# Kernel tuning notes

Hardware: AMD Instinct MI355X
Metric: run time of the kernel (lower is better)

The kernel has to match this reference:

```python
import jax, jax.numpy as jnp
import numpy as np

TEMPERATURE = 1.0
NEG_INF = -1e30  # finite stand-in for -inf: safe for log_softmax and its vjp


def setup_inputs() -> dict:
    key = jax.random.key(0)
    k1, k2 = jax.random.split(key)
    B, M, D = 4096, 3, 256
    tokens = jax.random.normal(k1, (B, M, D), dtype=jnp.float32)
    labels = jax.random.randint(k2, (B,), 0, 32, dtype=jnp.int32)
    return {"tokens": tokens, "labels": labels}


def reference(tokens, labels):
    # tokens: [B, M, D]; labels: [B]
    B, M, D = tokens.shape
    # Pairwise per-modality similarities: sim[i, k, m] = <tokens[i,m], tokens[k,m]>
    sim = jnp.einsum('imd,kmd->ikm', tokens, tokens) / TEMPERATURE
    self_mask = jnp.eye(B, dtype=bool)
    # Original excludes sample i itself from the candidate set; masking with a
    # huge negative logit makes it contribute 0 to the softmax partition.
    sim = jnp.where(self_mask[:, :, None], NEG_INF, sim)
    logp = jax.nn.log_softmax(sim, axis=1)  # softmax over the B-1 other samples

    # Positive pairs: same label, excluding self.
    pos = (labels[:, None] == labels[None, :]) & ~self_mask  # [B, B]
    pos_count = pos.sum(axis=1)                               # [B]
    valid = pos_count > 0                                     # sum(same_label) > 1

    # Mean log-prob over positives, per (sample, modality).
    pos_logp = jnp.einsum('ikm,ik->im', logp, pos.astype(logp.dtype))  # [B, M]
    denom = jnp.maximum(pos_count, 1).astype(logp.dtype)[:, None]
    per = jnp.where(valid[:, None], pos_logp / denom, 0.0)             # [B, M]

    num = valid.sum() * M
    return -per.sum() / num.astype(per.dtype)
```

## Files before the change

kernel.cpp:

```cpp
#include <hip/hip_runtime.h>

#define B_N 4096
#define M_N 3
#define D_N 256
#define LOG2E 1.44269504088896340736f
#define LN2   0.69314718055994530942f
#define C_OFF   64.0f
#define T_CLAMP 112.0f

typedef __bf16 bf16x8 __attribute__((ext_vector_type(8)));
typedef float  f32x4  __attribute__((ext_vector_type(4)));

__device__ __forceinline__ unsigned short f2bf(float f) {
    unsigned int u = __float_as_uint(f);
    u += 0x7FFFu + ((u >> 16) & 1u);
    return (unsigned short)(u >> 16);
}
__device__ __forceinline__ float bf2f(unsigned short h) {
    return __uint_as_float(((unsigned int)h) << 16);
}

__global__ void cvt_kernel(const float* __restrict__ in, unsigned short* __restrict__ out,
                           float* __restrict__ norm2) {
    int idx = blockIdx.x * blockDim.x + threadIdx.x;
    float4 v = reinterpret_cast<const float4*>(in)[idx];
    int i   = idx / 192;
    int rem = idx - i * 192;
    int m   = rem >> 6;
    int d4  = rem & 63;
    ushort4 o;
    o.x = f2bf(v.x); o.y = f2bf(v.y); o.z = f2bf(v.z); o.w = f2bf(v.w);
    reinterpret_cast<ushort4*>(out)[((size_t)m * B_N + i) * 64 + d4] = o;
    float nx = bf2f(o.x), ny = bf2f(o.y), nz = bf2f(o.z), nw = bf2f(o.w);
    float s = nx * nx + ny * ny + nz * nz + nw * nw;
#pragma unroll
    for (int msk = 1; msk < 64; msk <<= 1) s += __shfl_xor(s, msk);
    if ((threadIdx.x & 63) == 0) norm2[m * B_N + i] = s;
}

__global__ void hist_kernel(const int* __restrict__ labels, int* __restrict__ hist,
                            int* __restrict__ nvout) {
    __shared__ int h[32];
    __shared__ int nv;
    int tid = threadIdx.x;
    if (tid < 32) h[tid] = 0;
    if (tid == 0) nv = 0;
    __syncthreads();
    for (int i = tid; i < B_N; i += 256) atomicAdd(&h[labels[i]], 1);
    __syncthreads();
    int cnt = 0;
    for (int i = tid; i < B_N; i += 256) cnt += (h[labels[i]] >= 2) ? 1 : 0;
    atomicAdd(&nv, cnt);
    __syncthreads();
    if (tid < 32) hist[tid] = h[tid];
    if (tid == 0) nvout[0] = nv;
}

__global__ __launch_bounds__(256, 3) void main_kernel(
    const unsigned short* __restrict__ tokb, const int* __restrict__ labels,
    float2* __restrict__ partials) {
    int raw = blockIdx.x;
    int bid = (raw & 7) * 96 + (raw >> 3);
    int m  = bid >> 8;
    int ns = (bid >> 5) & 7;
    int rb = bid & 31;
    int i0 = rb * 128;
    int cb = ns * 512;

    int tid  = threadIdx.x;
    int wave = tid >> 6, lane = tid & 63;
    int lr = lane & 15, lk = lane >> 4;
    const unsigned short* tm = tokb + (size_t)m * (B_N * D_N);

    __shared__ __align__(16) char ldsB[2][8192];
    __shared__ int labl[512];
    labl[tid]       = labels[cb + tid];
    labl[tid + 256] = labels[cb + tid + 256];

    int r0 = i0 + wave * 32;
    bf16x8 afrag[2][8];
#pragma unroll
    for (int rt = 0; rt < 2; ++rt) {
        const unsigned short* rp = tm + (size_t)(r0 + rt * 16 + lr) * D_N + lk * 8;
#pragma unroll
        for (int kf = 0; kf < 8; ++kf)
            afrag[rt][kf] = *reinterpret_cast<const bf16x8*>(rp + kf * 32);
    }
    int labr[2][4];
#pragma unroll
    for (int rt = 0; rt < 2; ++rt)
#pragma unroll
        for (int j = 0; j < 4; ++j)
            labr[rt][j] = labels[r0 + rt * 16 + lk * 4 + j];

    float S[2][4] = {{0.f, 0.f, 0.f, 0.f}, {0.f, 0.f, 0.f, 0.f}};
    float P[2][4] = {{0.f, 0.f, 0.f, 0.f}, {0.f, 0.f, 0.f, 0.f}};

    int lc  = tid >> 5;
    int w   = tid & 31;
    int sch = w ^ (lc & 7);
    const unsigned short* sbase = tm + (size_t)(cb + lc) * D_N + sch * 8;

    {
        bf16x8 t0 = *reinterpret_cast<const bf16x8*>(sbase);
        bf16x8 t1 = *reinterpret_cast<const bf16x8*>(sbase + 8 * D_N);
        *reinterpret_cast<bf16x8*>(&ldsB[0][tid * 16])        = t0;
        *reinterpret_cast<bf16x8*>(&ldsB[0][4096 + tid * 16]) = t1;
    }

    for (int kb = 0; kb < 32; ++kb) {
        int cur = kb & 1;
        __syncthreads();

        int nkb = (kb + 1) & 31;
        const unsigned short* np = sbase + (size_t)nkb * (16 * D_N);
        bf16x8 nt0 = *reinterpret_cast<const bf16x8*>(np);
        bf16x8 nt1 = *reinterpret_cast<const bf16x8*>(np + 8 * D_N);

        const char* bp = ldsB[cur];
        int swz = (lr & 7) << 4;
        bf16x8 bfrag[8];
#pragma unroll
        for (int kf = 0; kf < 8; ++kf)
            bfrag[kf] = *reinterpret_cast<const bf16x8*>(
                bp + lr * 512 + ((((kf * 4 + lk) << 4)) ^ swz));
        int labc = labl[kb * 16 + lr];

        f32x4 acc0 = {0.f, 0.f, 0.f, 0.f};
        f32x4 acc1 = {0.f, 0.f, 0.f, 0.f};
#pragma unroll
        for (int kf = 0; kf < 8; ++kf) {
            acc0 = __builtin_amdgcn_mfma_f32_16x16x32_bf16(afrag[0][kf], bfrag[kf], acc0, 0, 0, 0);
            acc1 = __builtin_amdgcn_mfma_f32_16x16x32_bf16(afrag[1][kf], bfrag[kf], acc1, 0, 0, 0);
        }

        int cg0 = cb + kb * 16;
        if ((cg0 < r0 + 32) && (cg0 + 16 > r0)) {
            int colg = cg0 + lr;
#pragma unroll
            for (int rt = 0; rt < 2; ++rt) {
                f32x4 aa = rt ? acc1 : acc0;
#pragma unroll
                for (int j = 0; j < 4; ++j) {
                    float s = aa[j];
                    float t = fminf(fmaf(s, LOG2E, -C_OFF), T_CLAMP);
                    float e = __builtin_amdgcn_exp2f(t);
                    int row = r0 + rt * 16 + lk * 4 + j;
                    e = (colg == row) ? 0.f : e;
                    S[rt][j] += e;
                    P[rt][j] += (labc == labr[rt][j]) ? s : 0.f;
                }
            }
        } else {
#pragma unroll
            for (int rt = 0; rt < 2; ++rt) {
                f32x4 aa = rt ? acc1 : acc0;
#pragma unroll
                for (int j = 0; j < 4; ++j) {
                    float s = aa[j];
                    float t = fminf(fmaf(s, LOG2E, -C_OFF), T_CLAMP);
                    S[rt][j] += __builtin_amdgcn_exp2f(t);
                    P[rt][j] += (labc == labr[rt][j]) ? s : 0.f;
                }
            }
        }

        char* dst = (char*)ldsB[cur ^ 1];
        *reinterpret_cast<bf16x8*>(dst + tid * 16)        = nt0;
        *reinterpret_cast<bf16x8*>(dst + 4096 + tid * 16) = nt1;
    }

#pragma unroll
    for (int rt = 0; rt < 2; ++rt)
#pragma unroll
        for (int j = 0; j < 4; ++j) {
            float sv = S[rt][j], pv = P[rt][j];
#pragma unroll
            for (int msk = 1; msk < 16; msk <<= 1) {
                sv += __shfl_xor(sv, msk);
                pv += __shfl_xor(pv, msk);
            }
            if (lr == 0) {
                int rl = rt * 16 + lk * 4 + j;
                float2 q; q.x = sv; q.y = pv;
                partials[(size_t)(((m * 32 + rb) * 8 + ns) * 128) + wave * 32 + rl] = q;
            }
        }
}

__global__ void reduce_kernel(const float2* __restrict__ partials,
                              const float* __restrict__ norm2,
                              const int* __restrict__ labels,
                              const int* __restrict__ hist,
                              float* __restrict__ blockpart) {
    int gid = blockIdx.x * 256 + threadIdx.x;
    int m = gid >> 12, i = gid & 4095;
    int rb = i >> 7, r = i & 127;
    const float2* pp = partials + (size_t)(((m * 32 + rb) * 8) * 128) + r;
    float S = 0.f, P = 0.f;
#pragma unroll
    for (int ns = 0; ns < 8; ++ns) {
        float2 q = pp[ns * 128];
        S += q.x; P += q.y;
    }
    P -= norm2[gid];
    int pc = hist[labels[i]] - 1;
    float contrib = (pc > 0)
        ? (__builtin_amdgcn_logf(S) + C_OFF) * LN2 - P / (float)pc
        : 0.f;
#pragma unroll
    for (int off = 32; off >= 1; off >>= 1) contrib += __shfl_down(contrib, off);
    __shared__ float w4[4];
    if ((threadIdx.x & 63) == 0) w4[threadIdx.x >> 6] = contrib;
    __syncthreads();
    if (threadIdx.x == 0) blockpart[blockIdx.x] = w4[0] + w4[1] + w4[2] + w4[3];
}

__global__ void final_kernel(const float* __restrict__ blockpart, const int* __restrict__ nv,
                             float* __restrict__ out) {
    int lane = threadIdx.x;
    float s = (lane < 48) ? blockpart[lane] : 0.f;
#pragma unroll
    for (int off = 32; off >= 1; off >>= 1) s += __shfl_down(s, off);
    if (lane == 0) out[0] = s / (float)(nv[0] * M_N);
}

extern "C" void kernel_launch(void* const* d_in, const int* in_sizes, int n_in,
                              void* d_out, int out_size, void* d_ws, size_t ws_size,
                              hipStream_t stream) {
    const float* tokens = (const float*)d_in[0];
    const int*   labels = (const int*)d_in[1];
    float* out = (float*)d_out;

    char* ws = (char*)d_ws;
    int*    hist      = (int*)ws;
    int*    nv        = (int*)(ws + 128);
    float*  blockpart = (float*)(ws + 256);
    float*  norm2     = (float*)(ws + 1024);
    float2* partials  = (float2*)(ws + 65536);
    unsigned short* tokb = (unsigned short*)(ws + 1048576);

    cvt_kernel<<<3072, 256, 0, stream>>>(tokens, tokb, norm2);
    hist_kernel<<<1, 256, 0, stream>>>(labels, hist, nv);
    main_kernel<<<768, 256, 0, stream>>>(tokb, labels, partials);
    reduce_kernel<<<48, 256, 0, stream>>>(partials, norm2, labels, hist, blockpart);
    final_kernel<<<1, 64, 0, stream>>>(blockpart, nv, out);
}
```

Before: 56.91 us.

## Double LDS stage depth, add MFMA priority, drop exp clamp, widen hist block

The main kernel now stages 32 columns per LDS phase instead of 16, which halves the number of barriers per block and issues four global loads per thread per phase. It raises wave priority around the MFMA chains with s_setprio. It also removes the fminf clamp before exp2, and the histogram kernel runs with 1024 threads. Together these aim to cut barrier and instruction overhead, at the cost of doubled LDS use and a possible overflow if a similarity exceeds the clamp range.

```diff
diff --git a/kernel.cpp b/kernel.cpp
--- a/kernel.cpp
+++ b/kernel.cpp
@@ -5,8 +5,7 @@
 #define D_N 256
 #define LOG2E 1.44269504088896340736f
 #define LN2   0.69314718055994530942f
-#define C_OFF   64.0f
-#define T_CLAMP 112.0f
+#define C_OFF 64.0f
 
 typedef __bf16 bf16x8 __attribute__((ext_vector_type(8)));
 typedef float  f32x4  __attribute__((ext_vector_type(4)));
@@ -46,10 +45,10 @@
     if (tid < 32) h[tid] = 0;
     if (tid == 0) nv = 0;
     __syncthreads();
-    for (int i = tid; i < B_N; i += 256) atomicAdd(&h[labels[i]], 1);
+    for (int i = tid; i < B_N; i += 1024) atomicAdd(&h[labels[i]], 1);
     __syncthreads();
     int cnt = 0;
-    for (int i = tid; i < B_N; i += 256) cnt += (h[labels[i]] >= 2) ? 1 : 0;
+    for (int i = tid; i < B_N; i += 1024) cnt += (h[labels[i]] >= 2) ? 1 : 0;
     atomicAdd(&nv, cnt);
     __syncthreads();
     if (tid < 32) hist[tid] = h[tid];
@@ -72,7 +71,7 @@
     int lr = lane & 15, lk = lane >> 4;
     const unsigned short* tm = tokb + (size_t)m * (B_N * D_N);
 
-    __shared__ __align__(16) char ldsB[2][8192];
+    __shared__ __align__(16) char ldsB[2][16384];
     __shared__ int labl[512];
     labl[tid]       = labels[cb + tid];
     labl[tid + 256] = labels[cb + tid + 256];
@@ -104,70 +103,82 @@
     {
         bf16x8 t0 = *reinterpret_cast<const bf16x8*>(sbase);
         bf16x8 t1 = *reinterpret_cast<const bf16x8*>(sbase + 8 * D_N);
-        *reinterpret_cast<bf16x8*>(&ldsB[0][tid * 16])        = t0;
-        *reinterpret_cast<bf16x8*>(&ldsB[0][4096 + tid * 16]) = t1;
-    }
-
-    for (int kb = 0; kb < 32; ++kb) {
-        int cur = kb & 1;
+        bf16x8 t2 = *reinterpret_cast<const bf16x8*>(sbase + 16 * D_N);
+        bf16x8 t3 = *reinterpret_cast<const bf16x8*>(sbase + 24 * D_N);
+        *reinterpret_cast<bf16x8*>(&ldsB[0][tid * 16])         = t0;
+        *reinterpret_cast<bf16x8*>(&ldsB[0][4096 + tid * 16])  = t1;
+        *reinterpret_cast<bf16x8*>(&ldsB[0][8192 + tid * 16])  = t2;
+        *reinterpret_cast<bf16x8*>(&ldsB[0][12288 + tid * 16]) = t3;
+    }
+
+    for (int ph = 0; ph < 16; ++ph) {
+        int cur = ph & 1;
         __syncthreads();
 
-        int nkb = (kb + 1) & 31;
-        const unsigned short* np = sbase + (size_t)nkb * (16 * D_N);
+        int nph = (ph + 1) & 15;
+        const unsigned short* np = sbase + (size_t)nph * (32 * D_N);
         bf16x8 nt0 = *reinterpret_cast<const bf16x8*>(np);
         bf16x8 nt1 = *reinterpret_cast<const bf16x8*>(np + 8 * D_N);
+        bf16x8 nt2 = *reinterpret_cast<const bf16x8*>(np + 16 * D_N);
+        bf16x8 nt3 = *reinterpret_cast<const bf16x8*>(np + 24 * D_N);
 
         const char* bp = ldsB[cur];
         int swz = (lr & 7) << 4;
-        bf16x8 bfrag[8];
-#pragma unroll
-        for (int kf = 0; kf < 8; ++kf)
-            bfrag[kf] = *reinterpret_cast<const bf16x8*>(
-                bp + lr * 512 + ((((kf * 4 + lk) << 4)) ^ swz));
-        int labc = labl[kb * 16 + lr];
-
-        f32x4 acc0 = {0.f, 0.f, 0.f, 0.f};
-        f32x4 acc1 = {0.f, 0.f, 0.f, 0.f};
-#pragma unroll
-        for (int kf = 0; kf < 8; ++kf) {
-            acc0 = __builtin_amdgcn_mfma_f32_16x16x32_bf16(afrag[0][kf], bfrag[kf], acc0, 0, 0, 0);
-            acc1 = __builtin_amdgcn_mfma_f32_16x16x32_bf16(afrag[1][kf], bfrag[kf], acc1, 0, 0, 0);
+#pragma unroll
+        for (int s = 0; s < 2; ++s) {
+            bf16x8 bfrag[8];
+#pragma unroll
+            for (int kf = 0; kf < 8; ++kf)
+                bfrag[kf] = *reinterpret_cast<const bf16x8*>(
+                    bp + (s * 16 + lr) * 512 + (((kf * 4 + lk) << 4) ^ swz));
+            int kb = ph * 2 + s;
+            int labc = labl[kb * 16 + lr];
+
+            f32x4 acc0 = {0.f, 0.f, 0.f, 0.f};
+            f32x4 acc1 = {0.f, 0.f, 0.f, 0.f};
+            __builtin_amdgcn_s_setprio(1);
+#pragma unroll
+            for (int kf = 0; kf < 8; ++kf) {
+                acc0 = __builtin_amdgcn_mfma_f32_16x16x32_bf16(afrag[0][kf], bfrag[kf], acc0, 0, 0, 0);
+                acc1 = __builtin_amdgcn_mfma_f32_16x16x32_bf16(afrag[1][kf], bfrag[kf], acc1, 0, 0, 0);
+            }
+            __builtin_amdgcn_s_setprio(0);
+
+            int cg0 = cb + kb * 16;
+            if ((cg0 < r0 + 32) && (cg0 + 16 > r0)) {
+                int colg = cg0 + lr;
+#pragma unroll
+                for (int rt = 0; rt < 2; ++rt) {
+                    f32x4 aa = rt ? acc1 : acc0;
+#pragma unroll
+                    for (int j = 0; j < 4; ++j) {
+                        float s2 = aa[j];
+                        float e = __builtin_amdgcn_exp2f(fmaf(s2, LOG2E, -C_OFF));
+                        int row = r0 + rt * 16 + lk * 4 + j;
+                        e = (colg == row) ? 0.f : e;
+                        S[rt][j] += e;
+                        P[rt][j] += (labc == labr[rt][j]) ? s2 : 0.f;
+                    }
+                }
+            } else {
+#pragma unroll
+                for (int rt = 0; rt < 2; ++rt) {
+                    f32x4 aa = rt ? acc1 : acc0;
+#pragma unroll
+                    for (int j = 0; j < 4; ++j) {
+                        float s2 = aa[j];
+                        S[rt][j] += __builtin_amdgcn_exp2f(fmaf(s2, LOG2E, -C_OFF));
+                        P[rt][j] += (labc == labr[rt][j]) ? s2 : 0.f;
+                    }
+                }
+            }
         }
 
-        int cg0 = cb + kb * 16;
-        if ((cg0 < r0 + 32) && (cg0 + 16 > r0)) {
-            int colg = cg0 + lr;
-#pragma unroll
-            for (int rt = 0; rt < 2; ++rt) {
-                f32x4 aa = rt ? acc1 : acc0;
-#pragma unroll
-                for (int j = 0; j < 4; ++j) {
-                    float s = aa[j];
-                    float t = fminf(fmaf(s, LOG2E, -C_OFF), T_CLAMP);
-                    float e = __builtin_amdgcn_exp2f(t);
-                    int row = r0 + rt * 16 + lk * 4 + j;
-                    e = (colg == row) ? 0.f : e;
-                    S[rt][j] += e;
-                    P[rt][j] += (labc == labr[rt][j]) ? s : 0.f;
-                }
-            }
-        } else {
-#pragma unroll
-            for (int rt = 0; rt < 2; ++rt) {
-                f32x4 aa = rt ? acc1 : acc0;
-#pragma unroll
-                for (int j = 0; j < 4; ++j) {
-                    float s = aa[j];
-                    float t = fminf(fmaf(s, LOG2E, -C_OFF), T_CLAMP);
-                    S[rt][j] += __builtin_amdgcn_exp2f(t);
-                    P[rt][j] += (labc == labr[rt][j]) ? s : 0.f;
-                }
-            }
-        }
-
         char* dst = (char*)ldsB[cur ^ 1];
-        *reinterpret_cast<bf16x8*>(dst + tid * 16)        = nt0;
-        *reinterpret_cast<bf16x8*>(dst + 4096 + tid * 16) = nt1;
+        *reinterpret_cast<bf16x8*>(dst + tid * 16)         = nt0;
+        *reinterpret_cast<bf16x8*>(dst + 4096 + tid * 16)  = nt1;
+        *reinterpret_cast<bf16x8*>(dst + 8192 + tid * 16)  = nt2;
+        *reinterpret_cast<bf16x8*>(dst + 12288 + tid * 16) = nt3;
     }
 
 #pragma unroll
@@ -241,7 +252,7 @@
     unsigned short* tokb = (unsigned short*)(ws + 1048576);
 
     cvt_kernel<<<3072, 256, 0, stream>>>(tokens, tokb, norm2);
-    hist_kernel<<<1, 256, 0, stream>>>(labels, hist, nv);
+    hist_kernel<<<1, 1024, 0, stream>>>(labels, hist, nv);
     main_kernel<<<768, 256, 0, stream>>>(tokb, labels, partials);
     reduce_kernel<<<48, 256, 0, stream>>>(partials, norm2, labels, hist, blockpart);
     final_kernel<<<1, 64, 0, stream>>>(blockpart, nv, out);
```

After: 91.45 us. +60.7%, slower.
